# Kernel optimization log

Measured on AMD Instinct MI355X. Metric: run time of the kernel, lower is better.

Reference implementation:

```python
import jax, jax.numpy as jnp
import numpy as np

NUM_NODES = 200000
NUM_EDGES = 640000
RANK = 16
EMBED_DIM = 128


def setup_inputs() -> dict:
    key = jax.random.key(0)
    k1, k2, k3 = jax.random.split(key, 3)
    U = jax.random.normal(k1, (NUM_NODES, RANK), dtype=jnp.float32)
    V = jax.random.normal(k2, (RANK, EMBED_DIM), dtype=jnp.float32)
    edge_index = jax.random.randint(k3, (2, NUM_EDGES), 0, NUM_NODES, dtype=jnp.int64)
    return {"U": U, "V": V, "edge_index": edge_index}


def reference(U, V, edge_index):
    # Low-rank projection: [N, r] @ [r, d] -> [N, d]
    embeddings = jnp.matmul(U, V)
    src, dst = edge_index[0], edge_index[1]
    # Mean aggregation (PyG MessagePassing aggr='mean', source_to_target):
    # gather messages from source nodes, segment-mean into destination nodes.
    msgs = embeddings[src]  # [E, d]
    summed = jax.ops.segment_sum(msgs, dst, num_segments=NUM_NODES)  # [N, d]
    counts = jax.ops.segment_sum(jnp.ones((edge_index.shape[1],), dtype=embeddings.dtype),
                                 dst, num_segments=NUM_NODES)  # [N]
    denom = jnp.maximum(counts, 1.0)  # isolated nodes -> 0 output (scatter-mean semantics)
    return summed / denom[:, None]
```

## Files before the change

### kernel.cpp

```cpp
#include <hip/hip_runtime.h>
#include <hip/hip_bf16.h>

#define RANK 16
#define EMBED_DIM 128

__global__ void detect_idx_dtype(const unsigned int* __restrict__ words,
                                 int nwords, int* __restrict__ flag) {
    unsigned int v = 0;
    for (int i = threadIdx.x; i < 2048; i += 256) {
        int w = 2 * i + 1;
        if (w < nwords) v |= words[w];
    }
    if (__any(v != 0)) {
        if ((threadIdx.x & 63) == 0) atomicOr(flag, 1);
    }
}

__global__ void scatter_rank(const float* __restrict__ U,
                             const void* __restrict__ edge_index,
                             float* __restrict__ Usum,
                             float* __restrict__ counts,
                             const int* __restrict__ flag,
                             int E) {
    int gid = blockIdx.x * 256 + threadIdx.x;
    int e = gid >> 4;
    int j = gid & 15;
    if (e >= E) return;
    int src, dst;
    if (*flag) {
        const int* ei = (const int*)edge_index;
        src = ei[e];
        dst = ei[E + e];
    } else {
        const int* ei = (const int*)edge_index;
        src = ei[2 * e];
        dst = ei[2 * (E + e)];
    }
    atomicAdd(&Usum[(size_t)dst * RANK + j], U[(size_t)src * RANK + j]);
    if (j == 0) atomicAdd(&counts[dst], 1.0f);
}

__global__ __launch_bounds__(256) void project_out(
        const float* __restrict__ Usum,
        const float* __restrict__ counts,
        const float* __restrict__ V,
        float* __restrict__ out) {
    __shared__ float4 Vs4[RANK * EMBED_DIM / 4];
    int t = threadIdx.x;
    const float4* V4 = (const float4*)V;
    Vs4[t] = V4[t];
    Vs4[t + 256] = V4[t + 256];
    __syncthreads();

    int q = t & 31;
    int w = t >> 5;
    int n0 = blockIdx.x * 32 + 4 * w;

    const float4* Us4 = (const float4*)Usum;
    float4 a[4][4];
#pragma unroll
    for (int r = 0; r < 4; ++r)
#pragma unroll
        for (int k4 = 0; k4 < 4; ++k4)
            a[r][k4] = Us4[(size_t)(n0 + r) * 4 + k4];

    float4 acc[4];
#pragma unroll
    for (int r = 0; r < 4; ++r) acc[r] = make_float4(0.f, 0.f, 0.f, 0.f);

#pragma unroll
    for (int k = 0; k < RANK; ++k) {
        float4 v = Vs4[k * 32 + q];
#pragma unroll
        for (int r = 0; r < 4; ++r) {
            float ar = (k & 3) == 0 ? a[r][k >> 2].x
                     : (k & 3) == 1 ? a[r][k >> 2].y
                     : (k & 3) == 2 ? a[r][k >> 2].z
                                    : a[r][k >> 2].w;
            acc[r].x = fmaf(ar, v.x, acc[r].x);
            acc[r].y = fmaf(ar, v.y, acc[r].y);
            acc[r].z = fmaf(ar, v.z, acc[r].z);
            acc[r].w = fmaf(ar, v.w, acc[r].w);
        }
    }

    float4* out4 = (float4*)out;
#pragma unroll
    for (int r = 0; r < 4; ++r) {
        float c = counts[n0 + r];
        float s = 1.0f / fmaxf(c, 1.0f);
        out4[(size_t)(n0 + r) * (EMBED_DIM / 4) + q] =
            make_float4(acc[r].x * s, acc[r].y * s, acc[r].z * s, acc[r].w * s);
    }
}

extern "C" void kernel_launch(void* const* d_in, const int* in_sizes, int n_in,
                              void* d_out, int out_size, void* d_ws, size_t ws_size,
                              hipStream_t stream) {
    const float* U = (const float*)d_in[0];
    const float* V = (const float*)d_in[1];
    const void* EI = d_in[2];
    float* out = (float*)d_out;

    const int N = in_sizes[0] / RANK;
    const int E = in_sizes[2] / 2;

    float* Usum = (float*)d_ws;
    float* counts = Usum + (size_t)N * RANK;
    int* flag = (int*)(counts + N);
    size_t zero_bytes = ((size_t)N * RANK + N + 1) * sizeof(float);

    hipMemsetAsync(d_ws, 0, zero_bytes, stream);

    detect_idx_dtype<<<1, 256, 0, stream>>>((const unsigned int*)EI,
                                            in_sizes[2], flag);

    int scatter_threads = E * RANK;
    scatter_rank<<<(scatter_threads + 255) / 256, 256, 0, stream>>>(
        U, EI, Usum, counts, flag, E);

    project_out<<<N / 32, 256, 0, stream>>>(Usum, counts, V, out);
}
```

Measured before the change: 200.6 us.

## Replace float atomic scatter with CSR build and per-node gather fused with projection

Swaps the per-edge float atomicAdd scatter of rank-16 vectors for a CSR construction: integer histogram of destinations, three-pass prefix scan, and an atomic reorder of sources by destination. A fused kernel then gathers and sums U rows per destination node in registers, applies the mean and projects through V in shared memory. This removes 16 float atomics per edge and the zeroing and round trip of the Usum buffer. In exchange it adds several small kernel launches and serial per-node loops whose length depends on degree, and the summation order within each node is no longer fixed.

```diff
diff --git a/kernel.cpp b/kernel.cpp
--- a/kernel.cpp
+++ b/kernel.cpp
@@ -1,8 +1,8 @@
 #include <hip/hip_runtime.h>
-#include <hip/hip_bf16.h>
 
 #define RANK 16
 #define EMBED_DIM 128
+#define SCAN_TILE 1024
 
 __global__ void detect_idx_dtype(const unsigned int* __restrict__ words,
                                  int nwords, int* __restrict__ flag) {
@@ -16,81 +16,155 @@
     }
 }
 
-__global__ void scatter_rank(const float* __restrict__ U,
-                             const void* __restrict__ edge_index,
-                             float* __restrict__ Usum,
-                             float* __restrict__ counts,
-                             const int* __restrict__ flag,
-                             int E) {
-    int gid = blockIdx.x * 256 + threadIdx.x;
-    int e = gid >> 4;
-    int j = gid & 15;
+__global__ void edge_hist(const void* __restrict__ edge_index,
+                          int* __restrict__ off,
+                          const int* __restrict__ flag, int E) {
+    int e = blockIdx.x * 256 + threadIdx.x;
     if (e >= E) return;
+    const int* w = (const int*)edge_index;
+    int dst = *flag ? w[E + e] : w[2 * (E + e)];
+    atomicAdd(&off[dst], 1);
+}
+
+__global__ __launch_bounds__(256) void scan_pass1(int* __restrict__ off,
+                                                  int* __restrict__ bsums,
+                                                  int N) {
+    __shared__ int lds[256];
+    int t = threadIdx.x;
+    int base = blockIdx.x * SCAN_TILE + t * 4;
+    int c0 = 0, c1 = 0, c2 = 0, c3 = 0;
+    if (base + 3 < N) {
+        int4 v = *(const int4*)(off + base);
+        c0 = v.x; c1 = v.y; c2 = v.z; c3 = v.w;
+    } else {
+        if (base + 0 < N) c0 = off[base + 0];
+        if (base + 1 < N) c1 = off[base + 1];
+        if (base + 2 < N) c2 = off[base + 2];
+        if (base + 3 < N) c3 = off[base + 3];
+    }
+    int s = c0 + c1 + c2 + c3;
+    lds[t] = s;
+    __syncthreads();
+    for (int d = 1; d < 256; d <<= 1) {
+        int v = (t >= d) ? lds[t - d] : 0;
+        __syncthreads();
+        lds[t] += v;
+        __syncthreads();
+    }
+    int excl = lds[t] - s;
+    if (t == 255) bsums[blockIdx.x] = lds[255];
+    if (base + 3 < N) {
+        int4 o;
+        o.x = excl;
+        o.y = excl + c0;
+        o.z = excl + c0 + c1;
+        o.w = excl + c0 + c1 + c2;
+        *(int4*)(off + base) = o;
+    } else {
+        if (base + 0 < N) off[base + 0] = excl;
+        if (base + 1 < N) off[base + 1] = excl + c0;
+        if (base + 2 < N) off[base + 2] = excl + c0 + c1;
+        if (base + 3 < N) off[base + 3] = excl + c0 + c1 + c2;
+    }
+}
+
+__global__ __launch_bounds__(256) void scan_pass2(int* __restrict__ bsums,
+                                                  int NB) {
+    __shared__ int lds[256];
+    int t = threadIdx.x;
+    int s = (t < NB) ? bsums[t] : 0;
+    lds[t] = s;
+    __syncthreads();
+    for (int d = 1; d < 256; d <<= 1) {
+        int v = (t >= d) ? lds[t - d] : 0;
+        __syncthreads();
+        lds[t] += v;
+        __syncthreads();
+    }
+    if (t < NB) bsums[t] = lds[t] - s;
+}
+
+__global__ void scan_pass3(int* __restrict__ off, int* __restrict__ cur,
+                           const int* __restrict__ bsums, int N, int E) {
+    int i = blockIdx.x * 256 + threadIdx.x;
+    if (i == 0 && blockIdx.x == 0) off[N] = E;
+    if (i >= N) return;
+    int v = off[i] + bsums[i >> 10];
+    off[i] = v;
+    cur[i] = v;
+}
+
+__global__ void reorder_edges(const void* __restrict__ edge_index,
+                              int* __restrict__ cur, int* __restrict__ ssrc,
+                              const int* __restrict__ flag, int E) {
+    int e = blockIdx.x * 256 + threadIdx.x;
+    if (e >= E) return;
+    const int* w = (const int*)edge_index;
     int src, dst;
     if (*flag) {
-        const int* ei = (const int*)edge_index;
-        src = ei[e];
-        dst = ei[E + e];
+        src = w[e];
+        dst = w[E + e];
     } else {
-        const int* ei = (const int*)edge_index;
-        src = ei[2 * e];
-        dst = ei[2 * (E + e)];
-    }
-    atomicAdd(&Usum[(size_t)dst * RANK + j], U[(size_t)src * RANK + j]);
-    if (j == 0) atomicAdd(&counts[dst], 1.0f);
-}
-
-__global__ __launch_bounds__(256) void project_out(
-        const float* __restrict__ Usum,
-        const float* __restrict__ counts,
+        src = w[2 * e];
+        dst = w[2 * (E + e)];
+    }
+    int pos = atomicAdd(&cur[dst], 1);
+    ssrc[pos] = src;
+}
+
+__global__ __launch_bounds__(256) void gather_project(
+        const float* __restrict__ U,
         const float* __restrict__ V,
-        float* __restrict__ out) {
+        const int* __restrict__ off,
+        const int* __restrict__ ssrc,
+        float* __restrict__ out, int N) {
     __shared__ float4 Vs4[RANK * EMBED_DIM / 4];
+    __shared__ float accs[32][RANK];
+    __shared__ float sinv[32];
+
     int t = threadIdx.x;
     const float4* V4 = (const float4*)V;
     Vs4[t] = V4[t];
     Vs4[t + 256] = V4[t + 256];
+
+    int g = t >> 4;
+    int j = t & 15;
+#pragma unroll
+    for (int half = 0; half < 2; ++half) {
+        int nd = half * 16 + g;
+        int n = blockIdx.x * 32 + nd;
+        int o0 = 0, o1 = 0;
+        if (n < N) { o0 = off[n]; o1 = off[n + 1]; }
+        float acc = 0.f;
+        for (int e = o0; e < o1; ++e) {
+            int s = ssrc[e];
+            acc += U[(size_t)s * RANK + j];
+        }
+        accs[nd][j] = acc;
+        if (j == 0) sinv[nd] = 1.0f / fmaxf((float)(o1 - o0), 1.0f);
+    }
     __syncthreads();
 
     int q = t & 31;
     int w = t >> 5;
-    int n0 = blockIdx.x * 32 + 4 * w;
-
-    const float4* Us4 = (const float4*)Usum;
-    float4 a[4][4];
-#pragma unroll
-    for (int r = 0; r < 4; ++r)
-#pragma unroll
-        for (int k4 = 0; k4 < 4; ++k4)
-            a[r][k4] = Us4[(size_t)(n0 + r) * 4 + k4];
-
-    float4 acc[4];
-#pragma unroll
-    for (int r = 0; r < 4; ++r) acc[r] = make_float4(0.f, 0.f, 0.f, 0.f);
-
-#pragma unroll
-    for (int k = 0; k < RANK; ++k) {
-        float4 v = Vs4[k * 32 + q];
-#pragma unroll
-        for (int r = 0; r < 4; ++r) {
-            float ar = (k & 3) == 0 ? a[r][k >> 2].x
-                     : (k & 3) == 1 ? a[r][k >> 2].y
-                     : (k & 3) == 2 ? a[r][k >> 2].z
-                                    : a[r][k >> 2].w;
-            acc[r].x = fmaf(ar, v.x, acc[r].x);
-            acc[r].y = fmaf(ar, v.y, acc[r].y);
-            acc[r].z = fmaf(ar, v.z, acc[r].z);
-            acc[r].w = fmaf(ar, v.w, acc[r].w);
-        }
-    }
-
-    float4* out4 = (float4*)out;
 #pragma unroll
     for (int r = 0; r < 4; ++r) {
-        float c = counts[n0 + r];
-        float s = 1.0f / fmaxf(c, 1.0f);
-        out4[(size_t)(n0 + r) * (EMBED_DIM / 4) + q] =
-            make_float4(acc[r].x * s, acc[r].y * s, acc[r].z * s, acc[r].w * s);
+        int nd = 4 * w + r;
+        float4 acc4 = make_float4(0.f, 0.f, 0.f, 0.f);
+#pragma unroll
+        for (int k = 0; k < RANK; ++k) {
+            float a = accs[nd][k];
+            float4 v = Vs4[k * 32 + q];
+            acc4.x = fmaf(a, v.x, acc4.x);
+            acc4.y = fmaf(a, v.y, acc4.y);
+            acc4.z = fmaf(a, v.z, acc4.z);
+            acc4.w = fmaf(a, v.w, acc4.w);
+        }
+        float s = sinv[nd];
+        int n = blockIdx.x * 32 + nd;
+        if (n < N)
+            ((float4*)out)[(size_t)n * (EMBED_DIM / 4) + q] =
+                make_float4(acc4.x * s, acc4.y * s, acc4.z * s, acc4.w * s);
     }
 }
 
@@ -105,19 +179,25 @@
     const int N = in_sizes[0] / RANK;
     const int E = in_sizes[2] / 2;
 
-    float* Usum = (float*)d_ws;
-    float* counts = Usum + (size_t)N * RANK;
-    int* flag = (int*)(counts + N);
-    size_t zero_bytes = ((size_t)N * RANK + N + 1) * sizeof(float);
-
-    hipMemsetAsync(d_ws, 0, zero_bytes, stream);
+    int* off   = (int*)d_ws;
+    int* flag  = off + (N + 1);
+    int* cur   = flag + 1;
+    int* bsums = cur + N;
+    int* ssrc  = bsums + 256;
+
+    hipMemsetAsync(d_ws, 0, (size_t)(N + 2) * sizeof(int), stream);
 
     detect_idx_dtype<<<1, 256, 0, stream>>>((const unsigned int*)EI,
                                             in_sizes[2], flag);
 
-    int scatter_threads = E * RANK;
-    scatter_rank<<<(scatter_threads + 255) / 256, 256, 0, stream>>>(
-        U, EI, Usum, counts, flag, E);
-
-    project_out<<<N / 32, 256, 0, stream>>>(Usum, counts, V, out);
-}
+    edge_hist<<<(E + 255) / 256, 256, 0, stream>>>(EI, off, flag, E);
+
+    const int NB = (N + SCAN_TILE - 1) / SCAN_TILE;
+    scan_pass1<<<NB, 256, 0, stream>>>(off, bsums, N);
+    scan_pass2<<<1, 256, 0, stream>>>(bsums, NB);
+    scan_pass3<<<(N + 255) / 256, 256, 0, stream>>>(off, cur, bsums, N, E);
+
+    reorder_edges<<<(E + 255) / 256, 256, 0, stream>>>(EI, cur, ssrc, flag, E);
+
+    gather_project<<<(N + 31) / 32, 256, 0, stream>>>(U, V, off, ssrc, out, N);
+}
```

Measured after the change: 233.3 us. +16.4%, slower.

## Replace float atomic scatter with bucketed adjacency slots and gather-then-project

Applied to the files above, without the earlier changes.

Instead of 16 float atomicAdds per edge into a rank-16 sum buffer, each edge does a single integer atomic to claim a slot in a fixed-capacity (32) per-destination bucket, with an overflow list for high-degree nodes. A fused kernel then reads each node's source list, gathers and sums U rows, and projects through V in shared memory. The change removes float atomics, the large memset and the separate project pass. In exchange it adds a random slot write per edge, uninitialized slot reads for unused bucket entries (only the used ones are consumed), and a linear scan of the overflow list for any node whose degree exceeds the cap. The index dtype detection is folded into each block.

```diff
diff --git a/kernel.cpp b/kernel.cpp
--- a/kernel.cpp
+++ b/kernel.cpp
@@ -1,96 +1,132 @@
 #include <hip/hip_runtime.h>
-#include <hip/hip_bf16.h>
 
 #define RANK 16
 #define EMBED_DIM 128
+#define CAP 32
 
-__global__ void detect_idx_dtype(const unsigned int* __restrict__ words,
-                                 int nwords, int* __restrict__ flag) {
-    unsigned int v = 0;
-    for (int i = threadIdx.x; i < 2048; i += 256) {
-        int w = 2 * i + 1;
-        if (w < nwords) v |= words[w];
+__global__ __launch_bounds__(256) void fill_slots(
+        const int* __restrict__ eiw,
+        int* __restrict__ cnt,
+        int* __restrict__ ovfcnt,
+        int* __restrict__ slots,
+        int* __restrict__ ovf,
+        int E, int nwords) {
+    __shared__ int iflag;
+    if (threadIdx.x == 0) iflag = 0;
+    __syncthreads();
+    {
+        int w = 2 * threadIdx.x + 1;
+        unsigned int v = (w < nwords) ? ((const unsigned int*)eiw)[w] : 0u;
+        if (v) atomicOr(&iflag, 1);
     }
-    if (__any(v != 0)) {
-        if ((threadIdx.x & 63) == 0) atomicOr(flag, 1);
+    __syncthreads();
+    const bool is32 = (iflag != 0);
+
+    int e = blockIdx.x * 256 + threadIdx.x;
+    if (e >= E) return;
+    int src, dst;
+    if (is32) {
+        src = eiw[e];
+        dst = eiw[E + e];
+    } else {
+        src = eiw[2 * e];
+        dst = eiw[2 * (E + e)];
+    }
+    int pos = atomicAdd(&cnt[dst], 1);
+    if (pos < CAP) {
+        slots[(size_t)dst * CAP + pos] = src;
+    } else {
+        int o = atomicAdd(ovfcnt, 1);
+        ovf[2 * o]     = src;
+        ovf[2 * o + 1] = dst;
     }
 }
 
-__global__ void scatter_rank(const float* __restrict__ U,
-                             const void* __restrict__ edge_index,
-                             float* __restrict__ Usum,
-                             float* __restrict__ counts,
-                             const int* __restrict__ flag,
-                             int E) {
-    int gid = blockIdx.x * 256 + threadIdx.x;
-    int e = gid >> 4;
-    int j = gid & 15;
-    if (e >= E) return;
-    int src, dst;
-    if (*flag) {
-        const int* ei = (const int*)edge_index;
-        src = ei[e];
-        dst = ei[E + e];
-    } else {
-        const int* ei = (const int*)edge_index;
-        src = ei[2 * e];
-        dst = ei[2 * (E + e)];
+__global__ __launch_bounds__(256) void gather_project(
+        const float* __restrict__ U,
+        const float* __restrict__ V,
+        const int* __restrict__ cnt,
+        const int* __restrict__ slots,
+        const int* __restrict__ ovfcnt,
+        const int* __restrict__ ovf,
+        float* __restrict__ out, int N) {
+    __shared__ float4 Vs4[RANK * EMBED_DIM / 4];
+    __shared__ float accs[32][RANK];
+    __shared__ float sinv[32];
+    __shared__ int   scnt[32];
+    __shared__ int   sslot[32][CAP + 1];
+
+    const int t = threadIdx.x;
+    const float4* V4 = (const float4*)V;
+    Vs4[t]       = V4[t];
+    Vs4[t + 256] = V4[t + 256];
+
+    const int n0 = blockIdx.x * 32;
+
+    if (t < 32) {
+        int n = n0 + t;
+        int c = (n < N) ? cnt[n] : 0;
+        scnt[t] = c;
+        sinv[t] = 1.0f / fmaxf((float)c, 1.0f);
     }
-    atomicAdd(&Usum[(size_t)dst * RANK + j], U[(size_t)src * RANK + j]);
-    if (j == 0) atomicAdd(&counts[dst], 1.0f);
-}
-
-__global__ __launch_bounds__(256) void project_out(
-        const float* __restrict__ Usum,
-        const float* __restrict__ counts,
-        const float* __restrict__ V,
-        float* __restrict__ out) {
-    __shared__ float4 Vs4[RANK * EMBED_DIM / 4];
-    int t = threadIdx.x;
-    const float4* V4 = (const float4*)V;
-    Vs4[t] = V4[t];
-    Vs4[t + 256] = V4[t + 256];
+    {
+        const int4* g4 = (const int4*)(slots + (size_t)n0 * CAP);
+        int nd = t >> 3;
+        if (n0 + nd < N) {
+            int4 v = g4[t];
+            sslot[nd][(t & 7) * 4 + 0] = v.x;
+            sslot[nd][(t & 7) * 4 + 1] = v.y;
+            sslot[nd][(t & 7) * 4 + 2] = v.z;
+            sslot[nd][(t & 7) * 4 + 3] = v.w;
+        }
+    }
     __syncthreads();
 
-    int q = t & 31;
-    int w = t >> 5;
-    int n0 = blockIdx.x * 32 + 4 * w;
+    const int g = t >> 4;
+    const int j = t & 15;
+#pragma unroll
+    for (int half = 0; half < 2; ++half) {
+        int nd = half * 16 + g;
+        int n = n0 + nd;
+        float acc = 0.f;
+        if (n < N) {
+            int deg = scnt[nd];
+            int k = deg < CAP ? deg : CAP;
+            for (int e = 0; e < k; ++e) {
+                int s = sslot[nd][e];
+                acc += U[(size_t)s * RANK + j];
+            }
+            if (deg > CAP) {
+                int m = *ovfcnt;
+                for (int i = 0; i < m; ++i)
+                    if (ovf[2 * i + 1] == n)
+                        acc += U[(size_t)ovf[2 * i] * RANK + j];
+            }
+        }
+        accs[nd][j] = acc;
+    }
+    __syncthreads();
 
-    const float4* Us4 = (const float4*)Usum;
-    float4 a[4][4];
-#pragma unroll
-    for (int r = 0; r < 4; ++r)
-#pragma unroll
-        for (int k4 = 0; k4 < 4; ++k4)
-            a[r][k4] = Us4[(size_t)(n0 + r) * 4 + k4];
-
-    float4 acc[4];
-#pragma unroll
-    for (int r = 0; r < 4; ++r) acc[r] = make_float4(0.f, 0.f, 0.f, 0.f);
-
-#pragma unroll
-    for (int k = 0; k < RANK; ++k) {
-        float4 v = Vs4[k * 32 + q];
-#pragma unroll
-        for (int r = 0; r < 4; ++r) {
-            float ar = (k & 3) == 0 ? a[r][k >> 2].x
-                     : (k & 3) == 1 ? a[r][k >> 2].y
-                     : (k & 3) == 2 ? a[r][k >> 2].z
-                                    : a[r][k >> 2].w;
-            acc[r].x = fmaf(ar, v.x, acc[r].x);
-            acc[r].y = fmaf(ar, v.y, acc[r].y);
-            acc[r].z = fmaf(ar, v.z, acc[r].z);
-            acc[r].w = fmaf(ar, v.w, acc[r].w);
-        }
-    }
-
-    float4* out4 = (float4*)out;
+    const int q = t & 31;
+    const int w = t >> 5;
 #pragma unroll
     for (int r = 0; r < 4; ++r) {
-        float c = counts[n0 + r];
-        float s = 1.0f / fmaxf(c, 1.0f);
-        out4[(size_t)(n0 + r) * (EMBED_DIM / 4) + q] =
-            make_float4(acc[r].x * s, acc[r].y * s, acc[r].z * s, acc[r].w * s);
+        int nd = 4 * w + r;
+        float4 a4 = make_float4(0.f, 0.f, 0.f, 0.f);
+#pragma unroll
+        for (int k = 0; k < RANK; ++k) {
+            float a = accs[nd][k];
+            float4 v = Vs4[k * 32 + q];
+            a4.x = fmaf(a, v.x, a4.x);
+            a4.y = fmaf(a, v.y, a4.y);
+            a4.z = fmaf(a, v.z, a4.z);
+            a4.w = fmaf(a, v.w, a4.w);
+        }
+        float s = sinv[nd];
+        int n = n0 + nd;
+        if (n < N)
+            ((float4*)out)[(size_t)n * (EMBED_DIM / 4) + q] =
+                make_float4(a4.x * s, a4.y * s, a4.z * s, a4.w * s);
     }
 }
 
@@ -99,25 +135,25 @@
                               hipStream_t stream) {
     const float* U = (const float*)d_in[0];
     const float* V = (const float*)d_in[1];
-    const void* EI = d_in[2];
+    const int* EI = (const int*)d_in[2];
     float* out = (float*)d_out;
 
     const int N = in_sizes[0] / RANK;
     const int E = in_sizes[2] / 2;
+    const int nwords = in_sizes[2];
 
-    float* Usum = (float*)d_ws;
-    float* counts = Usum + (size_t)N * RANK;
-    int* flag = (int*)(counts + N);
-    size_t zero_bytes = ((size_t)N * RANK + N + 1) * sizeof(float);
+    int* wsI = (int*)d_ws;
+    int* cnt = wsI;
+    int* ovfcnt = wsI + N;
+    const int slots_off = (N + 1 + 15) & ~15;
+    int* slots = wsI + slots_off;
+    int* ovf = slots + (size_t)N * CAP;
 
-    hipMemsetAsync(d_ws, 0, zero_bytes, stream);
+    hipMemsetAsync(d_ws, 0, (size_t)(N + 1) * sizeof(int), stream);
 
-    detect_idx_dtype<<<1, 256, 0, stream>>>((const unsigned int*)EI,
-                                            in_sizes[2], flag);
+    fill_slots<<<(E + 255) / 256, 256, 0, stream>>>(
+        EI, cnt, ovfcnt, slots, ovf, E, nwords);
 
-    int scatter_threads = E * RANK;
-    scatter_rank<<<(scatter_threads + 255) / 256, 256, 0, stream>>>(
-        U, EI, Usum, counts, flag, E);
-
-    project_out<<<N / 32, 256, 0, stream>>>(Usum, counts, V, out);
+    gather_project<<<(N + 31) / 32, 256, 0, stream>>>(
+        U, V, cnt, slots, ovfcnt, ovf, out, N);
 }
```

Result: no change. 199.6 us (-0.5%).
